# Optimization experiments

Hardware: AMD Instinct MI355X
Metric: run time of the kernel (lower is better)

## Reference

```python
import jax, jax.numpy as jnp
import numpy as np

N_HEADS = 8
N_HIDDEN = 64  # out_features // n_heads
SLOPE = 0.2
NEG = -9e15


def setup_inputs() -> dict:
    key = jax.random.key(0)
    k1, k2, k3, k4, k5 = jax.random.split(key, 5)
    B, N, F_in, F_out = 4, 2048, 512, 512
    h = jax.random.normal(k1, (B, N, F_in), dtype=jnp.float32)
    adj = jax.random.randint(k2, (B, N, N), 0, 2, dtype=jnp.int32)
    # xavier_uniform with gain=1.414: limit = gain*sqrt(6/(fan_in+fan_out))
    lim_W = 1.414 * np.sqrt(6.0 / (F_in + F_out))
    W_l = jax.random.uniform(k3, (F_in, F_out), jnp.float32, -lim_W, lim_W)
    W_r = jax.random.uniform(k4, (F_in, F_out), jnp.float32, -lim_W, lim_W)
    lim_a = 1.414 * np.sqrt(6.0 / (N_HIDDEN + 1))
    a = jax.random.uniform(k5, (N_HIDDEN, 1), jnp.float32, -lim_a, lim_a)
    return {"h": h, "adj": adj, "W_l": W_l, "W_r": W_r, "a": a}


def reference(h, adj, W_l, W_r, a):
    B, N, _ = h.shape
    H, d = N_HEADS, N_HIDDEN
    # torch .view(-1, H, N, d) is a raw row-major reshape, replicated exactly here
    Wh_l = jax.nn.leaky_relu((h @ W_l).reshape(B, H, N, d), SLOPE)
    Wh_r = jax.nn.leaky_relu((h @ W_r).reshape(B, H, N, d), SLOPE)
    # e: [B,H,N,1] + [B,H,1,N] -> [B,H,N,N]
    e = Wh_l @ a + jnp.swapaxes(Wh_r @ a, 2, 3)
    att = jnp.where(adj[:, None, :, :] > 0, e, NEG)
    att = jax.nn.softmax(att, axis=-1)
    h_prime = att @ Wh_r  # [B,H,N,d]
    # torch .view(-1, N, H*d): raw reshape (no head transpose)
    out = jax.nn.elu(h_prime.reshape(B, N, H * d))
    return out
```

## Files before the change

kernel.cpp:

```cpp
#include <hip/hip_runtime.h>

#define NB   4
#define NN   2048
#define FIN  512
#define FOUT 512
#define NHD  8
#define DH   64
#define VTR  520
#define SLOPE 0.2f

typedef __attribute__((ext_vector_type(8)))  short bhalf8;
typedef __attribute__((ext_vector_type(16))) float f32x16;

__device__ __forceinline__ void load_lds16(const void* g, void* l) {
  __builtin_amdgcn_global_load_lds(
      (const __attribute__((address_space(1))) unsigned int*)g,
      (__attribute__((address_space(3))) unsigned int*)l, 16, 0, 0);
}

__device__ __forceinline__ unsigned short bfrne(float x) {
  unsigned int u = __float_as_uint(x);
  return (unsigned short)((u + 0x7FFFu + ((u >> 16) & 1u)) >> 16);
}

__device__ __forceinline__ void split2(float x, float y,
                                       unsigned int& hp, unsigned int& lp) {
  unsigned int ux = __float_as_uint(x), uy = __float_as_uint(y);
  unsigned int rx = (ux + 0x7FFFu + ((ux >> 16) & 1u)) & 0xFFFF0000u;
  unsigned int ry = (uy + 0x7FFFu + ((uy >> 16) & 1u)) & 0xFFFF0000u;
  float lx = x - __uint_as_float(rx);
  float ly = y - __uint_as_float(ry);
  unsigned int vx = __float_as_uint(lx), vy = __float_as_uint(ly);
  hp = (rx >> 16) | ry;
  lp = ((vx + 0x7FFFu + ((vx >> 16) & 1u)) >> 16)
     | ((vy + 0x7FFFu + ((vy >> 16) & 1u)) & 0xFFFF0000u);
}

__global__ __launch_bounds__(256) void k_split_prep(
    const float* __restrict__ h,
    unsigned short* __restrict__ hHi, unsigned short* __restrict__ hLo,
    const float* __restrict__ Wr,
    unsigned short* __restrict__ wTh, unsigned short* __restrict__ wTl)
{
  __shared__ float s[64][65];
  const int t = threadIdx.x;
  if (blockIdx.x < 2048) {
    size_t base = ((size_t)blockIdx.x * 256 + t) * 8;
    float4 a = *(const float4*)(h + base);
    float4 b = *(const float4*)(h + base + 4);
    uint4 uh, ul;
    split2(a.x, a.y, uh.x, ul.x);
    split2(a.z, a.w, uh.y, ul.y);
    split2(b.x, b.y, uh.z, ul.z);
    split2(b.z, b.w, uh.w, ul.w);
    *(uint4*)(hHi + base) = uh;
    *(uint4*)(hLo + base) = ul;
    return;
  }
  const int bid2 = blockIdx.x - 2048;
  const int n0 = (bid2 & 7) * 64, k0 = (bid2 >> 3) * 64;
#pragma unroll
  for (int p = 0; p < 4; ++p) {
    int row = p * 16 + (t >> 4);
    int col = (t & 15) * 4;
    float4 v = *(const float4*)(Wr + (size_t)(k0 + row) * FOUT + n0 + col);
    s[row][col] = v.x; s[row][col+1] = v.y; s[row][col+2] = v.z; s[row][col+3] = v.w;
  }
  __syncthreads();
  const int n = t >> 2;
  const int ks = (t & 3) * 16;
  uint4 h0, h1, l0, l1;
  split2(s[ks+ 0][n], s[ks+ 1][n], h0.x, l0.x);
  split2(s[ks+ 2][n], s[ks+ 3][n], h0.y, l0.y);
  split2(s[ks+ 4][n], s[ks+ 5][n], h0.z, l0.z);
  split2(s[ks+ 6][n], s[ks+ 7][n], h0.w, l0.w);
  split2(s[ks+ 8][n], s[ks+ 9][n], h1.x, l1.x);
  split2(s[ks+10][n], s[ks+11][n], h1.y, l1.y);
  split2(s[ks+12][n], s[ks+13][n], h1.z, l1.z);
  split2(s[ks+14][n], s[ks+15][n], h1.w, l1.w);
  size_t o = (size_t)(n0 + n) * FIN + k0 + ks;
  *(uint4*)(wTh + o) = h0; *(uint4*)(wTh + o + 8) = h1;
  *(uint4*)(wTl + o) = l0; *(uint4*)(wTl + o + 8) = l1;
}

__global__ __launch_bounds__(256) void k_gemm_whr_mfma(
    const unsigned short* __restrict__ hHi, const unsigned short* __restrict__ hLo,
    const unsigned short* __restrict__ wTh, const unsigned short* __restrict__ wTl,
    float* __restrict__ Whr, const float* __restrict__ av, float* __restrict__ er)
{
  __shared__ unsigned short sAh[128*64], sAl[128*64];
  __shared__ unsigned short sBh[64*64],  sBl[64*64];
  __shared__ float erT[128][2];
  const int tid = threadIdx.x, lane = tid & 63, wv = tid >> 6;
  const int Bid = blockIdx.x;
  const int g8 = Bid & 7, idx = Bid >> 3;
  const int sg = idx >> 3, ct = idx & 7;
  const int c0 = ct * 64;
  const int row0 = (g8 * 8 + sg) * 128;

  const unsigned short* pAh[4]; const unsigned short* pAl[4];
  unsigned short *dAh[4], *dAl[4];
#pragma unroll
  for (int t = 0; t < 4; ++t) {
    int I  = wv + t * 4;
    int rl = I * 8 + (lane >> 3);
    int gk = (lane & 7) ^ (rl & 7);
    pAh[t] = hHi + (size_t)(row0 + rl) * FIN + gk * 8;
    pAl[t] = hLo + (size_t)(row0 + rl) * FIN + gk * 8;
    dAh[t] = sAh + I * 512;  dAl[t] = sAl + I * 512;
  }
  const unsigned short* pBh[2]; const unsigned short* pBl[2];
  unsigned short *dBh[2], *dBl[2];
#pragma unroll
  for (int t = 0; t < 2; ++t) {
    int I  = wv + t * 4;
    int rl = I * 8 + (lane >> 3);
    int gk = (lane & 7) ^ (rl & 7);
    pBh[t] = wTh + (size_t)(c0 + rl) * FIN + gk * 8;
    pBl[t] = wTl + (size_t)(c0 + rl) * FIN + gk * 8;
    dBh[t] = sBh + I * 512;  dBl[t] = sBl + I * 512;
  }

  const int wi = wv >> 1, wc = wv & 1;
  const int l31 = lane & 31, half = lane >> 5;
  const int aoff0 = (wi*64 +      l31) * 64;
  const int aoff1 = (wi*64 + 32 + l31) * 64;
  const int boff  = (wc*32 +      l31) * 64;
  f32x16 acc0 = {}; f32x16 acc1 = {};

  for (int k0 = 0; k0 < FIN; k0 += 64) {
#pragma unroll
    for (int t = 0; t < 4; ++t) { load_lds16(pAh[t] + k0, dAh[t]);
                                  load_lds16(pAl[t] + k0, dAl[t]); }
#pragma unroll
    for (int t = 0; t < 2; ++t) { load_lds16(pBh[t] + k0, dBh[t]);
                                  load_lds16(pBl[t] + k0, dBl[t]); }
    __syncthreads();
#pragma unroll
    for (int kb = 0; kb < 4; ++kb) {
      int kg = ((kb*2 + half) ^ (lane & 7)) * 8;
      bhalf8 bh  = *(const bhalf8*)&sBh[boff  + kg];
      bhalf8 bl  = *(const bhalf8*)&sBl[boff  + kg];
      bhalf8 a0h = *(const bhalf8*)&sAh[aoff0 + kg];
      bhalf8 a0l = *(const bhalf8*)&sAl[aoff0 + kg];
      bhalf8 a1h = *(const bhalf8*)&sAh[aoff1 + kg];
      bhalf8 a1l = *(const bhalf8*)&sAl[aoff1 + kg];
      acc0 = __builtin_amdgcn_mfma_f32_32x32x16_bf16(a0h, bh, acc0, 0, 0, 0);
      acc1 = __builtin_amdgcn_mfma_f32_32x32x16_bf16(a1h, bh, acc1, 0, 0, 0);
      acc0 = __builtin_amdgcn_mfma_f32_32x32x16_bf16(a0l, bh, acc0, 0, 0, 0);
      acc1 = __builtin_amdgcn_mfma_f32_32x32x16_bf16(a1l, bh, acc1, 0, 0, 0);
      acc0 = __builtin_amdgcn_mfma_f32_32x32x16_bf16(a0h, bl, acc0, 0, 0, 0);
      acc1 = __builtin_amdgcn_mfma_f32_32x32x16_bf16(a1h, bl, acc1, 0, 0, 0);
    }
    __syncthreads();
  }

  const float a_d = av[wc*32 + l31];
#pragma unroll
  for (int mi = 0; mi < 2; ++mi) {
    const f32x16 a = mi ? acc1 : acc0;
#pragma unroll
    for (int reg = 0; reg < 16; ++reg) {
      int rmap = (reg & 3) + 8*(reg >> 2) + 4*half;
      int rowloc = wi*64 + mi*32 + rmap;
      int grow = row0 + rowloc;
      int b  = grow >> 11;
      int n  = grow & 2047;
      int hd = n >> 8;
      int jj = ((n & 255) << 3) | ct;
      float v = a[reg];
      v = v > 0.f ? v : SLOPE * v;
      Whr[(((size_t)(b*NHD + hd)) * NN + jj) * DH + (wc*32 + l31)] = v;
      float p = v * a_d;
      p += __shfl_xor(p, 16, 32);
      p += __shfl_xor(p,  8, 32);
      p += __shfl_xor(p,  4, 32);
      p += __shfl_xor(p,  2, 32);
      p += __shfl_xor(p,  1, 32);
      if (l31 == 0) erT[rowloc][wc] = p;
    }
  }
  __syncthreads();
  if (tid < 128) {
    int grow = row0 + tid;
    int b  = grow >> 11;
    int n  = grow & 2047;
    int hd = n >> 8;
    int jj = ((n & 255) << 3) | ct;
    er[((size_t)(b*NHD + hd)) * NN + jj] = erT[tid][0] + erT[tid][1];
  }
}

__global__ __launch_bounds__(256) void k_softvt(
    const float* __restrict__ Whr, const float* __restrict__ er,
    unsigned short* __restrict__ Vt)
{
  __shared__ float wm[4];
  __shared__ float wbuf[256];
  __shared__ unsigned short tile[64][264];
  const int tid = threadIdx.x;
  const int jc = blockIdx.x, hh = blockIdx.y, b = blockIdx.z;
  const float* ep = er + ((size_t)(b*NHD + hh)) * NN;
  float m = -1e30f;
  for (int j = tid; j < NN; j += 256) m = fmaxf(m, ep[j]);
#pragma unroll
  for (int off = 32; off; off >>= 1) m = fmaxf(m, __shfl_down(m, off, 64));
  if ((tid & 63) == 0) wm[tid >> 6] = m;
  __syncthreads();
  const float mm = fmaxf(fmaxf(wm[0], wm[1]), fmaxf(wm[2], wm[3]));
  const int j0 = jc * 256;
  float w = expf(ep[j0 + tid] - mm);
  wbuf[tid] = w;
  Vt[((size_t)(b*VTR + 512 + hh)) * NN + j0 + tid] = bfrne(w);
  __syncthreads();
  const size_t wbase = ((size_t)(b*NHD + hh)) * NN;
#pragma unroll
  for (int p = 0; p < 16; ++p) {
    int jr = p*16 + (tid >> 4);
    int dc = (tid & 15) * 4;
    float4 v = *(const float4*)(Whr + (wbase + j0 + jr) * DH + dc);
    float wj = wbuf[jr];
    tile[dc+0][jr] = bfrne(v.x * wj);
    tile[dc+1][jr] = bfrne(v.y * wj);
    tile[dc+2][jr] = bfrne(v.z * wj);
    tile[dc+3][jr] = bfrne(v.w * wj);
  }
  __syncthreads();
#pragma unroll
  for (int q = 0; q < 8; ++q) {
    int idx = q*256 + tid;
    int d = idx >> 5, seg = idx & 31;
    uint4 t16 = *(const uint4*)&tile[d][seg*8];
    *(uint4*)(Vt + ((size_t)(b*VTR + hh*64 + d)) * NN + j0 + seg*8) = t16;
  }
}

__global__ __launch_bounds__(256) void k_attn_out(
    const int* __restrict__ adj, const unsigned short* __restrict__ Vt,
    float* __restrict__ out)
{
  __shared__ unsigned short sA[128][72];
  __shared__ unsigned short sB[2][72*64];
  __shared__ float denL[128];
  const int tid = threadIdx.x;
  const int lane = tid & 63, wv = tid >> 6;
  const int Bid = blockIdx.x;
  const int g8 = Bid & 7, rest = Bid >> 3;
  const int ct = rest & 7, sg = rest >> 3;
  const int row0 = (g8*8 + sg) * 128;
  const int b = row0 >> 11;

  const unsigned short* pB[3];
  int dOff[3];
#pragma unroll
  for (int t = 0; t < 2; ++t) {
    int I  = wv + t*4;
    int rl = I*8 + (lane >> 3);
    int gk = (lane & 7) ^ (rl & 7);
    pB[t] = Vt + ((size_t)(b*VTR + ct*64 + rl))*NN + gk*8;
    dOff[t] = I*512;
  }
  {
    int x  = lane >> 3;
    int gk = (lane & 7) ^ (x & 7);
    pB[2] = Vt + ((size_t)(b*VTR + 512 + x))*NN + gk*8;
    dOff[2] = 64*64;
  }

  const int* adjp = adj + (size_t)b*NN*NN + (size_t)(row0 & 2047)*NN
                    + (tid >> 3)*NN + (tid & 7)*8;
  unsigned short* sAp = &sA[tid >> 3][(tid & 7)*8];

  const int wi = wv >> 1, wc = wv & 1;
  const int l31 = lane & 31, half = lane >> 5;
  f32x16 acc0 = {}; f32x16 acc1 = {}; f32x16 acc2 = {};
  const unsigned short* aRd0 = &sA[wi*64 +      l31][half*8];
  const unsigned short* aRd1 = &sA[wi*64 + 32 + l31][half*8];
  const int nloc = wc*32 + l31;

  load_lds16(pB[0], &sB[0][dOff[0]]);
  load_lds16(pB[1], &sB[0][dOff[1]]);
  if (wv == 0) load_lds16(pB[2], &sB[0][dOff[2]]);
  int4 q[8];
#pragma unroll
  for (int rr = 0; rr < 4; ++rr) {
    q[2*rr]   = *(const int4*)(adjp + rr*32*NN);
    q[2*rr+1] = *(const int4*)(adjp + rr*32*NN + 4);
  }

  for (int it = 0; it < 32; ++it) {
    const int cur = it & 1;
#pragma unroll
    for (int rr = 0; rr < 4; ++rr) {
      uint4 u;
      u.x = (unsigned)(q[2*rr].x   | (q[2*rr].y   << 16)) * 0x3F80u;
      u.y = (unsigned)(q[2*rr].z   | (q[2*rr].w   << 16)) * 0x3F80u;
      u.z = (unsigned)(q[2*rr+1].x | (q[2*rr+1].y << 16)) * 0x3F80u;
      u.w = (unsigned)(q[2*rr+1].z | (q[2*rr+1].w << 16)) * 0x3F80u;
      *(uint4*)(sAp + rr*32*72) = u;
    }
    __syncthreads();
    if (it < 31) {
      const int nk = (it + 1) * 64;
      unsigned short* nb = sB[cur ^ 1];
      load_lds16(pB[0] + nk, nb + dOff[0]);
      load_lds16(pB[1] + nk, nb + dOff[1]);
      if (wv == 0) load_lds16(pB[2] + nk, nb + dOff[2]);
#pragma unroll
      for (int rr = 0; rr < 4; ++rr) {
        q[2*rr]   = *(const int4*)(adjp + rr*32*NN + nk);
        q[2*rr+1] = *(const int4*)(adjp + rr*32*NN + nk + 4);
      }
    }
    const unsigned short* sBc = sB[cur];
#pragma unroll
    for (int kb = 0; kb < 4; ++kb) {
      int kg = (kb*2 + half) ^ (lane & 7);
      bhalf8 bf  = *(const bhalf8*)&sBc[nloc*64 + kg*8];
      bhalf8 bf2 = {};
      if (l31 < 8) bf2 = *(const bhalf8*)&sBc[(64 + l31)*64 + kg*8];
      bhalf8 a0 = *(const bhalf8*)(aRd0 + kb*16);
      bhalf8 a1 = *(const bhalf8*)(aRd1 + kb*16);
      acc0 = __builtin_amdgcn_mfma_f32_32x32x16_bf16(a0, bf,  acc0, 0, 0, 0);
      acc1 = __builtin_amdgcn_mfma_f32_32x32x16_bf16(a1, bf,  acc1, 0, 0, 0);
      acc2 = __builtin_amdgcn_mfma_f32_32x32x16_bf16(wc ? a1 : a0, bf2, acc2, 0, 0, 0);
    }
    __syncthreads();
  }
  if (l31 == ct) {
#pragma unroll
    for (int reg = 0; reg < 16; ++reg)
      denL[wv*32 + (reg & 3) + 8*(reg >> 2) + 4*half] = acc2[reg];
  }
  __syncthreads();
  const int ib = row0 & 2047;
#pragma unroll
  for (int mi = 0; mi < 2; ++mi) {
    const f32x16 a = mi ? acc1 : acc0;
#pragma unroll
    for (int reg = 0; reg < 16; ++reg) {
      int il = wi*64 + mi*32 + (reg & 3) + 8*(reg >> 2) + 4*half;
      int i  = ib + il;
      float v = a[reg] / denL[il];
      v = v > 0.f ? v : expm1f(v);
      int n = (ct << 8) | (i >> 3);
      int f = ((i & 7) << 6) | nloc;
      out[((size_t)b*NN + n)*FOUT + f] = v;
    }
  }
}

extern "C" void kernel_launch(void* const* d_in, const int* in_sizes, int n_in,
                              void* d_out, int out_size, void* d_ws, size_t ws_size,
                              hipStream_t stream)
{
  const float* hin = (const float*)d_in[0];
  const int*   adj = (const int*)d_in[1];
  const float* Wr  = (const float*)d_in[3];
  const float* av  = (const float*)d_in[4];
  float* out = (float*)d_out;

  char* ws = (char*)d_ws;
  unsigned short* hHi = (unsigned short*)(ws);
  unsigned short* hLo = (unsigned short*)(ws + 8388608);
  unsigned short* wTh = (unsigned short*)(ws + 16777216);
  unsigned short* wTl = (unsigned short*)(ws + 17301504);
  float* Whr  = (float*)(ws + 17825792);
  float* er   = (float*)(ws + 34603008);
  unsigned short* Vt = (unsigned short*)(ws);

  k_split_prep   <<<dim3(2112),    256, 0, stream>>>(hin, hHi, hLo, Wr, wTh, wTl);
  k_gemm_whr_mfma<<<dim3(512),     256, 0, stream>>>(hHi, hLo, wTh, wTl, Whr, av, er);
  k_softvt       <<<dim3(8, 8, 4), 256, 0, stream>>>(Whr, er, Vt);
  k_attn_out     <<<dim3(512),     256, 0, stream>>>(adj, Vt, out);
}
```

Measured before the change: 198.6 us.

## Fuse four kernels into one persistent kernel with software grid barriers

Merges the split/prep, GEMM, softmax-weight and attention kernels into one 512-block kernel whose stages share an LDS union and are separated by atomic-counter grid barriers. The aim is to remove inter-kernel launch gaps and tail drain between stages. The softmax stage now uses 128-column chunks so its work maps onto the same 512 blocks. The barrier needs all 512 blocks co-resident (launch_bounds 256,2) and adds a memset launch plus spin-wait cost at each stage boundary.

```diff
diff --git a/kernel.cpp b/kernel.cpp
--- a/kernel.cpp
+++ b/kernel.cpp
@@ -8,6 +8,7 @@
 #define DH   64
 #define VTR  520
 #define SLOPE 0.2f
+#define NBLK 512
 
 typedef __attribute__((ext_vector_type(8)))  short bhalf8;
 typedef __attribute__((ext_vector_type(16))) float f32x16;
@@ -36,316 +37,340 @@
      | ((vy + 0x7FFFu + ((vy >> 16) & 1u)) & 0xFFFF0000u);
 }
 
-__global__ __launch_bounds__(256) void k_split_prep(
-    const float* __restrict__ h,
-    unsigned short* __restrict__ hHi, unsigned short* __restrict__ hLo,
-    const float* __restrict__ Wr,
-    unsigned short* __restrict__ wTh, unsigned short* __restrict__ wTl)
-{
-  __shared__ float s[64][65];
-  const int t = threadIdx.x;
-  if (blockIdx.x < 2048) {
-    size_t base = ((size_t)blockIdx.x * 256 + t) * 8;
-    float4 a = *(const float4*)(h + base);
-    float4 b = *(const float4*)(h + base + 4);
-    uint4 uh, ul;
-    split2(a.x, a.y, uh.x, ul.x);
-    split2(a.z, a.w, uh.y, ul.y);
-    split2(b.x, b.y, uh.z, ul.z);
-    split2(b.z, b.w, uh.w, ul.w);
-    *(uint4*)(hHi + base) = uh;
-    *(uint4*)(hLo + base) = ul;
-    return;
-  }
-  const int bid2 = blockIdx.x - 2048;
-  const int n0 = (bid2 & 7) * 64, k0 = (bid2 >> 3) * 64;
-#pragma unroll
-  for (int p = 0; p < 4; ++p) {
-    int row = p * 16 + (t >> 4);
-    int col = (t & 15) * 4;
-    float4 v = *(const float4*)(Wr + (size_t)(k0 + row) * FOUT + n0 + col);
-    s[row][col] = v.x; s[row][col+1] = v.y; s[row][col+2] = v.z; s[row][col+3] = v.w;
+union SharedMem {
+  struct { float s[64][65]; } prep;
+  struct {
+    unsigned short sAh[128*64], sAl[128*64];
+    unsigned short sBh[64*64],  sBl[64*64];
+    float erT[128][2];
+  } gemm;
+  struct { float wm[4]; float wbuf[128]; unsigned short tile[64][136]; } soft;
+  struct {
+    unsigned short sA[128][72];
+    unsigned short sB[2][72*64];
+    float denL[128];
+  } attn;
+};
+
+__device__ __forceinline__ void grid_sync(unsigned* bar) {
+  __syncthreads();
+  if (threadIdx.x == 0) {
+    __threadfence();
+    unsigned g = __hip_atomic_load(&bar[1], __ATOMIC_RELAXED, __HIP_MEMORY_SCOPE_AGENT);
+    unsigned a = __hip_atomic_fetch_add(&bar[0], 1u, __ATOMIC_ACQ_REL, __HIP_MEMORY_SCOPE_AGENT);
+    if (a + 1u == (unsigned)NBLK) {
+      __hip_atomic_store(&bar[0], 0u, __ATOMIC_RELAXED, __HIP_MEMORY_SCOPE_AGENT);
+      __hip_atomic_fetch_add(&bar[1], 1u, __ATOMIC_RELEASE, __HIP_MEMORY_SCOPE_AGENT);
+    } else {
+      while (__hip_atomic_load(&bar[1], __ATOMIC_ACQUIRE, __HIP_MEMORY_SCOPE_AGENT) == g)
+        __builtin_amdgcn_s_sleep(8);
+    }
   }
   __syncthreads();
-  const int n = t >> 2;
-  const int ks = (t & 3) * 16;
-  uint4 h0, h1, l0, l1;
-  split2(s[ks+ 0][n], s[ks+ 1][n], h0.x, l0.x);
-  split2(s[ks+ 2][n], s[ks+ 3][n], h0.y, l0.y);
-  split2(s[ks+ 4][n], s[ks+ 5][n], h0.z, l0.z);
-  split2(s[ks+ 6][n], s[ks+ 7][n], h0.w, l0.w);
-  split2(s[ks+ 8][n], s[ks+ 9][n], h1.x, l1.x);
-  split2(s[ks+10][n], s[ks+11][n], h1.y, l1.y);
-  split2(s[ks+12][n], s[ks+13][n], h1.z, l1.z);
-  split2(s[ks+14][n], s[ks+15][n], h1.w, l1.w);
-  size_t o = (size_t)(n0 + n) * FIN + k0 + ks;
-  *(uint4*)(wTh + o) = h0; *(uint4*)(wTh + o + 8) = h1;
-  *(uint4*)(wTl + o) = l0; *(uint4*)(wTl + o + 8) = l1;
-}
-
-__global__ __launch_bounds__(256) void k_gemm_whr_mfma(
-    const unsigned short* __restrict__ hHi, const unsigned short* __restrict__ hLo,
-    const unsigned short* __restrict__ wTh, const unsigned short* __restrict__ wTl,
-    float* __restrict__ Whr, const float* __restrict__ av, float* __restrict__ er)
+}
+
+__global__ __launch_bounds__(256, 2) void k_fused(
+    const float* __restrict__ hin, const int* __restrict__ adj,
+    const float* __restrict__ Wr,  const float* __restrict__ av,
+    float* __restrict__ out,
+    unsigned short* __restrict__ hHi, unsigned short* __restrict__ hLo,
+    unsigned short* __restrict__ wTh, unsigned short* __restrict__ wTl,
+    float* __restrict__ Whr, float* __restrict__ er,
+    unsigned short* __restrict__ Vt, unsigned* __restrict__ bar)
 {
-  __shared__ unsigned short sAh[128*64], sAl[128*64];
-  __shared__ unsigned short sBh[64*64],  sBl[64*64];
-  __shared__ float erT[128][2];
-  const int tid = threadIdx.x, lane = tid & 63, wv = tid >> 6;
-  const int Bid = blockIdx.x;
-  const int g8 = Bid & 7, idx = Bid >> 3;
-  const int sg = idx >> 3, ct = idx & 7;
-  const int c0 = ct * 64;
-  const int row0 = (g8 * 8 + sg) * 128;
-
-  const unsigned short* pAh[4]; const unsigned short* pAl[4];
-  unsigned short *dAh[4], *dAl[4];
-#pragma unroll
-  for (int t = 0; t < 4; ++t) {
-    int I  = wv + t * 4;
-    int rl = I * 8 + (lane >> 3);
-    int gk = (lane & 7) ^ (rl & 7);
-    pAh[t] = hHi + (size_t)(row0 + rl) * FIN + gk * 8;
-    pAl[t] = hLo + (size_t)(row0 + rl) * FIN + gk * 8;
-    dAh[t] = sAh + I * 512;  dAl[t] = sAl + I * 512;
+  __shared__ SharedMem smem;
+  const int tid = threadIdx.x;
+  const int bid = blockIdx.x;
+  const int lane = tid & 63, wv = tid >> 6;
+
+  for (int u = bid; u < 2112; u += NBLK) {
+    if (u < 2048) {
+      size_t base = ((size_t)u * 256 + tid) * 8;
+      float4 a = *(const float4*)(hin + base);
+      float4 b = *(const float4*)(hin + base + 4);
+      uint4 uh, ul;
+      split2(a.x, a.y, uh.x, ul.x);
+      split2(a.z, a.w, uh.y, ul.y);
+      split2(b.x, b.y, uh.z, ul.z);
+      split2(b.z, b.w, uh.w, ul.w);
+      *(uint4*)(hHi + base) = uh;
+      *(uint4*)(hLo + base) = ul;
+    } else {
+      auto& s = smem.prep.s;
+      const int bid2 = u - 2048;
+      const int n0 = (bid2 & 7) * 64, k0 = (bid2 >> 3) * 64;
+#pragma unroll
+      for (int p = 0; p < 4; ++p) {
+        int row = p * 16 + (tid >> 4);
+        int col = (tid & 15) * 4;
+        float4 v = *(const float4*)(Wr + (size_t)(k0 + row) * FOUT + n0 + col);
+        s[row][col] = v.x; s[row][col+1] = v.y; s[row][col+2] = v.z; s[row][col+3] = v.w;
+      }
+      __syncthreads();
+      const int n = tid >> 2;
+      const int ks = (tid & 3) * 16;
+      uint4 h0, h1, l0, l1;
+      split2(s[ks+ 0][n], s[ks+ 1][n], h0.x, l0.x);
+      split2(s[ks+ 2][n], s[ks+ 3][n], h0.y, l0.y);
+      split2(s[ks+ 4][n], s[ks+ 5][n], h0.z, l0.z);
+      split2(s[ks+ 6][n], s[ks+ 7][n], h0.w, l0.w);
+      split2(s[ks+ 8][n], s[ks+ 9][n], h1.x, l1.x);
+      split2(s[ks+10][n], s[ks+11][n], h1.y, l1.y);
+      split2(s[ks+12][n], s[ks+13][n], h1.z, l1.z);
+      split2(s[ks+14][n], s[ks+15][n], h1.w, l1.w);
+      size_t o = (size_t)(n0 + n) * FIN + k0 + ks;
+      *(uint4*)(wTh + o) = h0; *(uint4*)(wTh + o + 8) = h1;
+      *(uint4*)(wTl + o) = l0; *(uint4*)(wTl + o + 8) = l1;
+    }
   }
-  const unsigned short* pBh[2]; const unsigned short* pBl[2];
-  unsigned short *dBh[2], *dBl[2];
-#pragma unroll
-  for (int t = 0; t < 2; ++t) {
-    int I  = wv + t * 4;
-    int rl = I * 8 + (lane >> 3);
-    int gk = (lane & 7) ^ (rl & 7);
-    pBh[t] = wTh + (size_t)(c0 + rl) * FIN + gk * 8;
-    pBl[t] = wTl + (size_t)(c0 + rl) * FIN + gk * 8;
-    dBh[t] = sBh + I * 512;  dBl[t] = sBl + I * 512;
-  }
-
-  const int wi = wv >> 1, wc = wv & 1;
-  const int l31 = lane & 31, half = lane >> 5;
-  const int aoff0 = (wi*64 +      l31) * 64;
-  const int aoff1 = (wi*64 + 32 + l31) * 64;
-  const int boff  = (wc*32 +      l31) * 64;
-  f32x16 acc0 = {}; f32x16 acc1 = {};
-
-  for (int k0 = 0; k0 < FIN; k0 += 64) {
-#pragma unroll
-    for (int t = 0; t < 4; ++t) { load_lds16(pAh[t] + k0, dAh[t]);
-                                  load_lds16(pAl[t] + k0, dAl[t]); }
-#pragma unroll
-    for (int t = 0; t < 2; ++t) { load_lds16(pBh[t] + k0, dBh[t]);
-                                  load_lds16(pBl[t] + k0, dBl[t]); }
+  grid_sync(bar);
+
+  {
+    auto& S = smem.gemm;
+    const int g8 = bid & 7, idx = bid >> 3;
+    const int sg = idx >> 3, ct = idx & 7;
+    const int c0 = ct * 64;
+    const int row0 = (g8 * 8 + sg) * 128;
+
+    const unsigned short* pAh[4]; const unsigned short* pAl[4];
+    unsigned short *dAh[4], *dAl[4];
+#pragma unroll
+    for (int t = 0; t < 4; ++t) {
+      int I  = wv + t * 4;
+      int rl = I * 8 + (lane >> 3);
+      int gk = (lane & 7) ^ (rl & 7);
+      pAh[t] = hHi + (size_t)(row0 + rl) * FIN + gk * 8;
+      pAl[t] = hLo + (size_t)(row0 + rl) * FIN + gk * 8;
+      dAh[t] = S.sAh + I * 512;  dAl[t] = S.sAl + I * 512;
+    }
+    const unsigned short* pBh[2]; const unsigned short* pBl[2];
+    unsigned short *dBh[2], *dBl[2];
+#pragma unroll
+    for (int t = 0; t < 2; ++t) {
+      int I  = wv + t * 4;
+      int rl = I * 8 + (lane >> 3);
+      int gk = (lane & 7) ^ (rl & 7);
+      pBh[t] = wTh + (size_t)(c0 + rl) * FIN + gk * 8;
+      pBl[t] = wTl + (size_t)(c0 + rl) * FIN + gk * 8;
+      dBh[t] = S.sBh + I * 512;  dBl[t] = S.sBl + I * 512;
+    }
+
+    const int wi = wv >> 1, wc = wv & 1;
+    const int l31 = lane & 31, half = lane >> 5;
+    const int aoff0 = (wi*64 +      l31) * 64;
+    const int aoff1 = (wi*64 + 32 + l31) * 64;
+    const int boff  = (wc*32 +      l31) * 64;
+    f32x16 acc0 = {}; f32x16 acc1 = {};
+
+    for (int k0 = 0; k0 < FIN; k0 += 64) {
+#pragma unroll
+      for (int t = 0; t < 4; ++t) { load_lds16(pAh[t] + k0, dAh[t]);
+                                    load_lds16(pAl[t] + k0, dAl[t]); }
+#pragma unroll
+      for (int t = 0; t < 2; ++t) { load_lds16(pBh[t] + k0, dBh[t]);
+                                    load_lds16(pBl[t] + k0, dBl[t]); }
+      __syncthreads();
+#pragma unroll
+      for (int kb = 0; kb < 4; ++kb) {
+        int kg = ((kb*2 + half) ^ (lane & 7)) * 8;
+        bhalf8 bh  = *(const bhalf8*)&S.sBh[boff  + kg];
+        bhalf8 bl  = *(const bhalf8*)&S.sBl[boff  + kg];
+        bhalf8 a0h = *(const bhalf8*)&S.sAh[aoff0 + kg];
+        bhalf8 a0l = *(const bhalf8*)&S.sAl[aoff0 + kg];
+        bhalf8 a1h = *(const bhalf8*)&S.sAh[aoff1 + kg];
+        bhalf8 a1l = *(const bhalf8*)&S.sAl[aoff1 + kg];
+        acc0 = __builtin_amdgcn_mfma_f32_32x32x16_bf16(a0h, bh, acc0, 0, 0, 0);
+        acc1 = __builtin_amdgcn_mfma_f32_32x32x16_bf16(a1h, bh, acc1, 0, 0, 0);
+        acc0 = __builtin_amdgcn_mfma_f32_32x32x16_bf16(a0l, bh, acc0, 0, 0, 0);
+        acc1 = __builtin_amdgcn_mfma_f32_32x32x16_bf16(a1l, bh, acc1, 0, 0, 0);
+        acc0 = __builtin_amdgcn_mfma_f32_32x32x16_bf16(a0h, bl, acc0, 0, 0, 0);
+        acc1 = __builtin_amdgcn_mfma_f32_32x32x16_bf16(a1h, bl, acc1, 0, 0, 0);
+      }
+      __syncthreads();
+    }
+
+    const float a_d = av[wc*32 + l31];
+#pragma unroll
+    for (int mi = 0; mi < 2; ++mi) {
+      const f32x16 a = mi ? acc1 : acc0;
+#pragma unroll
+      for (int reg = 0; reg < 16; ++reg) {
+        int rmap = (reg & 3) + 8*(reg >> 2) + 4*half;
+        int rowloc = wi*64 + mi*32 + rmap;
+        int grow = row0 + rowloc;
+        int b  = grow >> 11;
+        int n  = grow & 2047;
+        int hd = n >> 8;
+        int jj = ((n & 255) << 3) | ct;
+        float v = a[reg];
+        v = v > 0.f ? v : SLOPE * v;
+        Whr[(((size_t)(b*NHD + hd)) * NN + jj) * DH + (wc*32 + l31)] = v;
+        float p = v * a_d;
+        p += __shfl_xor(p, 16, 32);
+        p += __shfl_xor(p,  8, 32);
+        p += __shfl_xor(p,  4, 32);
+        p += __shfl_xor(p,  2, 32);
+        p += __shfl_xor(p,  1, 32);
+        if (l31 == 0) S.erT[rowloc][wc] = p;
+      }
+    }
     __syncthreads();
-#pragma unroll
-    for (int kb = 0; kb < 4; ++kb) {
-      int kg = ((kb*2 + half) ^ (lane & 7)) * 8;
-      bhalf8 bh  = *(const bhalf8*)&sBh[boff  + kg];
-      bhalf8 bl  = *(const bhalf8*)&sBl[boff  + kg];
-      bhalf8 a0h = *(const bhalf8*)&sAh[aoff0 + kg];
-      bhalf8 a0l = *(const bhalf8*)&sAl[aoff0 + kg];
-      bhalf8 a1h = *(const bhalf8*)&sAh[aoff1 + kg];
-      bhalf8 a1l = *(const bhalf8*)&sAl[aoff1 + kg];
-      acc0 = __builtin_amdgcn_mfma_f32_32x32x16_bf16(a0h, bh, acc0, 0, 0, 0);
-      acc1 = __builtin_amdgcn_mfma_f32_32x32x16_bf16(a1h, bh, acc1, 0, 0, 0);
-      acc0 = __builtin_amdgcn_mfma_f32_32x32x16_bf16(a0l, bh, acc0, 0, 0, 0);
-      acc1 = __builtin_amdgcn_mfma_f32_32x32x16_bf16(a1l, bh, acc1, 0, 0, 0);
-      acc0 = __builtin_amdgcn_mfma_f32_32x32x16_bf16(a0h, bl, acc0, 0, 0, 0);
-      acc1 = __builtin_amdgcn_mfma_f32_32x32x16_bf16(a1h, bl, acc1, 0, 0, 0);
-    }
-    __syncthreads();
-  }
-
-  const float a_d = av[wc*32 + l31];
-#pragma unroll
-  for (int mi = 0; mi < 2; ++mi) {
-    const f32x16 a = mi ? acc1 : acc0;
-#pragma unroll
-    for (int reg = 0; reg < 16; ++reg) {
-      int rmap = (reg & 3) + 8*(reg >> 2) + 4*half;
-      int rowloc = wi*64 + mi*32 + rmap;
-      int grow = row0 + rowloc;
+    if (tid < 128) {
+      int grow = row0 + tid;
       int b  = grow >> 11;
       int n  = grow & 2047;
       int hd = n >> 8;
       int jj = ((n & 255) << 3) | ct;
-      float v = a[reg];
-      v = v > 0.f ? v : SLOPE * v;
-      Whr[(((size_t)(b*NHD + hd)) * NN + jj) * DH + (wc*32 + l31)] = v;
-      float p = v * a_d;
-      p += __shfl_xor(p, 16, 32);
-      p += __shfl_xor(p,  8, 32);
-      p += __shfl_xor(p,  4, 32);
-      p += __shfl_xor(p,  2, 32);
-      p += __shfl_xor(p,  1, 32);
-      if (l31 == 0) erT[rowloc][wc] = p;
+      er[((size_t)(b*NHD + hd)) * NN + jj] = S.erT[tid][0] + S.erT[tid][1];
     }
   }
-  __syncthreads();
-  if (tid < 128) {
-    int grow = row0 + tid;
-    int b  = grow >> 11;
-    int n  = grow & 2047;
-    int hd = n >> 8;
-    int jj = ((n & 255) << 3) | ct;
-    er[((size_t)(b*NHD + hd)) * NN + jj] = erT[tid][0] + erT[tid][1];
+  grid_sync(bar);
+
+  {
+    auto& S = smem.soft;
+    const int jc = bid & 15, hh = (bid >> 4) & 7, b = bid >> 7;
+    const float* ep = er + ((size_t)(b*NHD + hh)) * NN;
+    float m = -1e30f;
+    for (int j = tid; j < NN; j += 256) m = fmaxf(m, ep[j]);
+#pragma unroll
+    for (int off = 32; off; off >>= 1) m = fmaxf(m, __shfl_down(m, off, 64));
+    if ((tid & 63) == 0) S.wm[tid >> 6] = m;
+    __syncthreads();
+    const float mm = fmaxf(fmaxf(S.wm[0], S.wm[1]), fmaxf(S.wm[2], S.wm[3]));
+    const int j0 = jc * 128;
+    if (tid < 128) {
+      float w = expf(ep[j0 + tid] - mm);
+      S.wbuf[tid] = w;
+      Vt[((size_t)(b*VTR + 512 + hh)) * NN + j0 + tid] = bfrne(w);
+    }
+    __syncthreads();
+    const size_t wbase = ((size_t)(b*NHD + hh)) * NN;
+#pragma unroll
+    for (int p = 0; p < 8; ++p) {
+      int jr = p*16 + (tid >> 4);
+      int dc = (tid & 15) * 4;
+      float4 v = *(const float4*)(Whr + (wbase + j0 + jr) * DH + dc);
+      float wj = S.wbuf[jr];
+      S.tile[dc+0][jr] = bfrne(v.x * wj);
+      S.tile[dc+1][jr] = bfrne(v.y * wj);
+      S.tile[dc+2][jr] = bfrne(v.z * wj);
+      S.tile[dc+3][jr] = bfrne(v.w * wj);
+    }
+    __syncthreads();
+#pragma unroll
+    for (int q = 0; q < 4; ++q) {
+      int idx = q*256 + tid;
+      int d = idx >> 4, seg = idx & 15;
+      uint4 t16 = *(const uint4*)&S.tile[d][seg*8];
+      *(uint4*)(Vt + ((size_t)(b*VTR + hh*64 + d)) * NN + j0 + seg*8) = t16;
+    }
   }
-}
-
-__global__ __launch_bounds__(256) void k_softvt(
-    const float* __restrict__ Whr, const float* __restrict__ er,
-    unsigned short* __restrict__ Vt)
-{
-  __shared__ float wm[4];
-  __shared__ float wbuf[256];
-  __shared__ unsigned short tile[64][264];
-  const int tid = threadIdx.x;
-  const int jc = blockIdx.x, hh = blockIdx.y, b = blockIdx.z;
-  const float* ep = er + ((size_t)(b*NHD + hh)) * NN;
-  float m = -1e30f;
-  for (int j = tid; j < NN; j += 256) m = fmaxf(m, ep[j]);
-#pragma unroll
-  for (int off = 32; off; off >>= 1) m = fmaxf(m, __shfl_down(m, off, 64));
-  if ((tid & 63) == 0) wm[tid >> 6] = m;
-  __syncthreads();
-  const float mm = fmaxf(fmaxf(wm[0], wm[1]), fmaxf(wm[2], wm[3]));
-  const int j0 = jc * 256;
-  float w = expf(ep[j0 + tid] - mm);
-  wbuf[tid] = w;
-  Vt[((size_t)(b*VTR + 512 + hh)) * NN + j0 + tid] = bfrne(w);
-  __syncthreads();
-  const size_t wbase = ((size_t)(b*NHD + hh)) * NN;
-#pragma unroll
-  for (int p = 0; p < 16; ++p) {
-    int jr = p*16 + (tid >> 4);
-    int dc = (tid & 15) * 4;
-    float4 v = *(const float4*)(Whr + (wbase + j0 + jr) * DH + dc);
-    float wj = wbuf[jr];
-    tile[dc+0][jr] = bfrne(v.x * wj);
-    tile[dc+1][jr] = bfrne(v.y * wj);
-    tile[dc+2][jr] = bfrne(v.z * wj);
-    tile[dc+3][jr] = bfrne(v.w * wj);
-  }
-  __syncthreads();
-#pragma unroll
-  for (int q = 0; q < 8; ++q) {
-    int idx = q*256 + tid;
-    int d = idx >> 5, seg = idx & 31;
-    uint4 t16 = *(const uint4*)&tile[d][seg*8];
-    *(uint4*)(Vt + ((size_t)(b*VTR + hh*64 + d)) * NN + j0 + seg*8) = t16;
-  }
-}
-
-__global__ __launch_bounds__(256) void k_attn_out(
-    const int* __restrict__ adj, const unsigned short* __restrict__ Vt,
-    float* __restrict__ out)
-{
-  __shared__ unsigned short sA[128][72];
-  __shared__ unsigned short sB[2][72*64];
-  __shared__ float denL[128];
-  const int tid = threadIdx.x;
-  const int lane = tid & 63, wv = tid >> 6;
-  const int Bid = blockIdx.x;
-  const int g8 = Bid & 7, rest = Bid >> 3;
-  const int ct = rest & 7, sg = rest >> 3;
-  const int row0 = (g8*8 + sg) * 128;
-  const int b = row0 >> 11;
-
-  const unsigned short* pB[3];
-  int dOff[3];
-#pragma unroll
-  for (int t = 0; t < 2; ++t) {
-    int I  = wv + t*4;
-    int rl = I*8 + (lane >> 3);
-    int gk = (lane & 7) ^ (rl & 7);
-    pB[t] = Vt + ((size_t)(b*VTR + ct*64 + rl))*NN + gk*8;
-    dOff[t] = I*512;
-  }
+  grid_sync(bar);
+
   {
-    int x  = lane >> 3;
-    int gk = (lane & 7) ^ (x & 7);
-    pB[2] = Vt + ((size_t)(b*VTR + 512 + x))*NN + gk*8;
-    dOff[2] = 64*64;
-  }
-
-  const int* adjp = adj + (size_t)b*NN*NN + (size_t)(row0 & 2047)*NN
-                    + (tid >> 3)*NN + (tid & 7)*8;
-  unsigned short* sAp = &sA[tid >> 3][(tid & 7)*8];
-
-  const int wi = wv >> 1, wc = wv & 1;
-  const int l31 = lane & 31, half = lane >> 5;
-  f32x16 acc0 = {}; f32x16 acc1 = {}; f32x16 acc2 = {};
-  const unsigned short* aRd0 = &sA[wi*64 +      l31][half*8];
-  const unsigned short* aRd1 = &sA[wi*64 + 32 + l31][half*8];
-  const int nloc = wc*32 + l31;
-
-  load_lds16(pB[0], &sB[0][dOff[0]]);
-  load_lds16(pB[1], &sB[0][dOff[1]]);
-  if (wv == 0) load_lds16(pB[2], &sB[0][dOff[2]]);
-  int4 q[8];
-#pragma unroll
-  for (int rr = 0; rr < 4; ++rr) {
-    q[2*rr]   = *(const int4*)(adjp + rr*32*NN);
-    q[2*rr+1] = *(const int4*)(adjp + rr*32*NN + 4);
-  }
-
-  for (int it = 0; it < 32; ++it) {
-    const int cur = it & 1;
+    auto& S = smem.attn;
+    const int g8 = bid & 7, rest = bid >> 3;
+    const int ct = rest & 7, sg = rest >> 3;
+    const int row0 = (g8*8 + sg) * 128;
+    const int b = row0 >> 11;
+
+    const unsigned short* pB[3];
+    int dOff[3];
+#pragma unroll
+    for (int t = 0; t < 2; ++t) {
+      int I  = wv + t*4;
+      int rl = I*8 + (lane >> 3);
+      int gk = (lane & 7) ^ (rl & 7);
+      pB[t] = Vt + ((size_t)(b*VTR + ct*64 + rl))*NN + gk*8;
+      dOff[t] = I*512;
+    }
+    {
+      int x  = lane >> 3;
+      int gk = (lane & 7) ^ (x & 7);
+      pB[2] = Vt + ((size_t)(b*VTR + 512 + x))*NN + gk*8;
+      dOff[2] = 64*64;
+    }
+
+    const int* adjp = adj + (size_t)b*NN*NN + (size_t)(row0 & 2047)*NN
+                      + (tid >> 3)*NN + (tid & 7)*8;
+    unsigned short* sAp = &S.sA[tid >> 3][(tid & 7)*8];
+
+    const int wi = wv >> 1, wc = wv & 1;
+    const int l31 = lane & 31, half = lane >> 5;
+    f32x16 acc0 = {}; f32x16 acc1 = {}; f32x16 acc2 = {};
+    const unsigned short* aRd0 = &S.sA[wi*64 +      l31][half*8];
+    const unsigned short* aRd1 = &S.sA[wi*64 + 32 + l31][half*8];
+    const int nloc = wc*32 + l31;
+
+    load_lds16(pB[0], &S.sB[0][dOff[0]]);
+    load_lds16(pB[1], &S.sB[0][dOff[1]]);
+    if (wv == 0) load_lds16(pB[2], &S.sB[0][dOff[2]]);
+    int4 q[8];
 #pragma unroll
     for (int rr = 0; rr < 4; ++rr) {
-      uint4 u;
-      u.x = (unsigned)(q[2*rr].x   | (q[2*rr].y   << 16)) * 0x3F80u;
-      u.y = (unsigned)(q[2*rr].z   | (q[2*rr].w   << 16)) * 0x3F80u;
-      u.z = (unsigned)(q[2*rr+1].x | (q[2*rr+1].y << 16)) * 0x3F80u;
-      u.w = (unsigned)(q[2*rr+1].z | (q[2*rr+1].w << 16)) * 0x3F80u;
-      *(uint4*)(sAp + rr*32*72) = u;
+      q[2*rr]   = *(const int4*)(adjp + rr*32*NN);
+      q[2*rr+1] = *(const int4*)(adjp + rr*32*NN + 4);
+    }
+
+    for (int it = 0; it < 32; ++it) {
+      const int cur = it & 1;
+#pragma unroll
+      for (int rr = 0; rr < 4; ++rr) {
+        uint4 u;
+        u.x = (unsigned)(q[2*rr].x   | (q[2*rr].y   << 16)) * 0x3F80u;
+        u.y = (unsigned)(q[2*rr].z   | (q[2*rr].w   << 16)) * 0x3F80u;
+        u.z = (unsigned)(q[2*rr+1].x | (q[2*rr+1].y << 16)) * 0x3F80u;
+        u.w = (unsigned)(q[2*rr+1].z | (q[2*rr+1].w << 16)) * 0x3F80u;
+        *(uint4*)(sAp + rr*32*72) = u;
+      }
+      __syncthreads();
+      if (it < 31) {
+        const int nk = (it + 1) * 64;
+        unsigned short* nb = S.sB[cur ^ 1];
+        load_lds16(pB[0] + nk, nb + dOff[0]);
+        load_lds16(pB[1] + nk, nb + dOff[1]);
+        if (wv == 0) load_lds16(pB[2] + nk, nb + dOff[2]);
+#pragma unroll
+        for (int rr = 0; rr < 4; ++rr) {
+          q[2*rr]   = *(const int4*)(adjp + rr*32*NN + nk);
+          q[2*rr+1] = *(const int4*)(adjp + rr*32*NN + nk + 4);
+        }
+      }
+      const unsigned short* sBc = S.sB[cur];
+#pragma unroll
+      for (int kb = 0; kb < 4; ++kb) {
+        int kg = (kb*2 + half) ^ (lane & 7);
+        bhalf8 bf  = *(const bhalf8*)&sBc[nloc*64 + kg*8];
+        bhalf8 bf2 = {};
+        if (l31 < 8) bf2 = *(const bhalf8*)&sBc[(64 + l31)*64 + kg*8];
+        bhalf8 a0 = *(const bhalf8*)(aRd0 + kb*16);
+        bhalf8 a1 = *(const bhalf8*)(aRd1 + kb*16);
+        acc0 = __builtin_amdgcn_mfma_f32_32x32x16_bf16(a0, bf,  acc0, 0, 0, 0);
+        acc1 = __builtin_amdgcn_mfma_f32_32x32x16_bf16(a1, bf,  acc1, 0, 0, 0);
+        acc2 = __builtin_amdgcn_mfma_f32_32x32x16_bf16(wc ? a1 : a0, bf2, acc2, 0, 0, 0);
+      }
+      __syncthreads();
+    }
+    if (l31 == ct) {
+#pragma unroll
+      for (int reg = 0; reg < 16; ++reg)
+        S.denL[wv*32 + (reg & 3) + 8*(reg >> 2) + 4*half] = acc2[reg];
     }
     __syncthreads();
-    if (it < 31) {
-      const int nk = (it + 1) * 64;
-      unsigned short* nb = sB[cur ^ 1];
-      load_lds16(pB[0] + nk, nb + dOff[0]);
-      load_lds16(pB[1] + nk, nb + dOff[1]);
-      if (wv == 0) load_lds16(pB[2] + nk, nb + dOff[2]);
-#pragma unroll
-      for (int rr = 0; rr < 4; ++rr) {
-        q[2*rr]   = *(const int4*)(adjp + rr*32*NN + nk);
-        q[2*rr+1] = *(const int4*)(adjp + rr*32*NN + nk + 4);
-      }
-    }
-    const unsigned short* sBc = sB[cur];
-#pragma unroll
-    for (int kb = 0; kb < 4; ++kb) {
-      int kg = (kb*2 + half) ^ (lane & 7);
-      bhalf8 bf  = *(const bhalf8*)&sBc[nloc*64 + kg*8];
-      bhalf8 bf2 = {};
-      if (l31 < 8) bf2 = *(const bhalf8*)&sBc[(64 + l31)*64 + kg*8];
-      bhalf8 a0 = *(const bhalf8*)(aRd0 + kb*16);
-      bhalf8 a1 = *(const bhalf8*)(aRd1 + kb*16);
-      acc0 = __builtin_amdgcn_mfma_f32_32x32x16_bf16(a0, bf,  acc0, 0, 0, 0);
-      acc1 = __builtin_amdgcn_mfma_f32_32x32x16_bf16(a1, bf,  acc1, 0, 0, 0);
-      acc2 = __builtin_amdgcn_mfma_f32_32x32x16_bf16(wc ? a1 : a0, bf2, acc2, 0, 0, 0);
-    }
-    __syncthreads();
-  }
-  if (l31 == ct) {
-#pragma unroll
-    for (int reg = 0; reg < 16; ++reg)
-      denL[wv*32 + (reg & 3) + 8*(reg >> 2) + 4*half] = acc2[reg];
-  }
-  __syncthreads();
-  const int ib = row0 & 2047;
-#pragma unroll
-  for (int mi = 0; mi < 2; ++mi) {
-    const f32x16 a = mi ? acc1 : acc0;
-#pragma unroll
-    for (int reg = 0; reg < 16; ++reg) {
-      int il = wi*64 + mi*32 + (reg & 3) + 8*(reg >> 2) + 4*half;
-      int i  = ib + il;
-      float v = a[reg] / denL[il];
-      v = v > 0.f ? v : expm1f(v);
-      int n = (ct << 8) | (i >> 3);
-      int f = ((i & 7) << 6) | nloc;
-      out[((size_t)b*NN + n)*FOUT + f] = v;
+    const int ib = row0 & 2047;
+#pragma unroll
+    for (int mi = 0; mi < 2; ++mi) {
+      const f32x16 a = mi ? acc1 : acc0;
+#pragma unroll
+      for (int reg = 0; reg < 16; ++reg) {
+        int il = wi*64 + mi*32 + (reg & 3) + 8*(reg >> 2) + 4*half;
+        int i  = ib + il;
+        float v = a[reg] / S.denL[il];
+        v = v > 0.f ? v : expm1f(v);
+        int n = (ct << 8) | (i >> 3);
+        int f = ((i & 7) << 6) | nloc;
+        out[((size_t)b*NN + n)*FOUT + f] = v;
+      }
     }
   }
 }
@@ -368,9 +393,9 @@
   float* Whr  = (float*)(ws + 17825792);
   float* er   = (float*)(ws + 34603008);
   unsigned short* Vt = (unsigned short*)(ws);
-
-  k_split_prep   <<<dim3(2112),    256, 0, stream>>>(hin, hHi, hLo, Wr, wTh, wTl);
-  k_gemm_whr_mfma<<<dim3(512),     256, 0, stream>>>(hHi, hLo, wTh, wTl, Whr, av, er);
-  k_softvt       <<<dim3(8, 8, 4), 256, 0, stream>>>(Whr, er, Vt);
-  k_attn_out     <<<dim3(512),     256, 0, stream>>>(adj, Vt, out);
-}
+  unsigned* bar = (unsigned*)(ws + 34865152);
+
+  hipMemsetAsync(bar, 0, 8, stream);
+  k_fused<<<dim3(NBLK), dim3(256), 0, stream>>>(
+      hin, adj, Wr, av, out, hHi, hLo, wTh, wTl, Whr, er, Vt, bar);
+}
```

New measurement: 429.8 us. 116% more time.

## Halve attention row tile to 64 rows and store Whr intermediate as bf16

Applied to the files above, without the earlier changes.

The attention-output kernel now handles 64 rows per block instead of 128 and launches twice as many blocks. Each wave keeps one accumulator, and the denominator MFMA runs only on half the waves. Launch bounds ask for four blocks per CU, aiming at better occupancy and latency hiding. Separately, the Whr intermediate is written as bf16 rather than fp32, halving its write and read traffic between the GEMM and softvt kernels. This adds an extra rounding step, and each Vt tile is now loaded twice as often across blocks.

```diff
diff --git a/kernel.cpp b/kernel.cpp
--- a/kernel.cpp
+++ b/kernel.cpp
@@ -21,6 +21,9 @@
 __device__ __forceinline__ unsigned short bfrne(float x) {
   unsigned int u = __float_as_uint(x);
   return (unsigned short)((u + 0x7FFFu + ((u >> 16) & 1u)) >> 16);
+}
+__device__ __forceinline__ float bf2f(unsigned short u) {
+  return __uint_as_float(((unsigned int)u) << 16);
 }
 
 __device__ __forceinline__ void split2(float x, float y,
@@ -86,7 +89,8 @@
 __global__ __launch_bounds__(256) void k_gemm_whr_mfma(
     const unsigned short* __restrict__ hHi, const unsigned short* __restrict__ hLo,
     const unsigned short* __restrict__ wTh, const unsigned short* __restrict__ wTl,
-    float* __restrict__ Whr, const float* __restrict__ av, float* __restrict__ er)
+    unsigned short* __restrict__ Whr, const float* __restrict__ av,
+    float* __restrict__ er)
 {
   __shared__ unsigned short sAh[128*64], sAl[128*64];
   __shared__ unsigned short sBh[64*64],  sBl[64*64];
@@ -170,7 +174,7 @@
       int jj = ((n & 255) << 3) | ct;
       float v = a[reg];
       v = v > 0.f ? v : SLOPE * v;
-      Whr[(((size_t)(b*NHD + hd)) * NN + jj) * DH + (wc*32 + l31)] = v;
+      Whr[(((size_t)(b*NHD + hd)) * NN + jj) * DH + (wc*32 + l31)] = bfrne(v);
       float p = v * a_d;
       p += __shfl_xor(p, 16, 32);
       p += __shfl_xor(p,  8, 32);
@@ -192,7 +196,7 @@
 }
 
 __global__ __launch_bounds__(256) void k_softvt(
-    const float* __restrict__ Whr, const float* __restrict__ er,
+    const unsigned short* __restrict__ Whr, const float* __restrict__ er,
     unsigned short* __restrict__ Vt)
 {
   __shared__ float wm[4];
@@ -218,12 +222,12 @@
   for (int p = 0; p < 16; ++p) {
     int jr = p*16 + (tid >> 4);
     int dc = (tid & 15) * 4;
-    float4 v = *(const float4*)(Whr + (wbase + j0 + jr) * DH + dc);
+    ushort4 v = *(const ushort4*)(Whr + (wbase + j0 + jr) * DH + dc);
     float wj = wbuf[jr];
-    tile[dc+0][jr] = bfrne(v.x * wj);
-    tile[dc+1][jr] = bfrne(v.y * wj);
-    tile[dc+2][jr] = bfrne(v.z * wj);
-    tile[dc+3][jr] = bfrne(v.w * wj);
+    tile[dc+0][jr] = bfrne(bf2f(v.x) * wj);
+    tile[dc+1][jr] = bfrne(bf2f(v.y) * wj);
+    tile[dc+2][jr] = bfrne(bf2f(v.z) * wj);
+    tile[dc+3][jr] = bfrne(bf2f(v.w) * wj);
   }
   __syncthreads();
 #pragma unroll
@@ -235,19 +239,19 @@
   }
 }
 
-__global__ __launch_bounds__(256) void k_attn_out(
+__global__ __launch_bounds__(256, 4) void k_attn_out(
     const int* __restrict__ adj, const unsigned short* __restrict__ Vt,
     float* __restrict__ out)
 {
-  __shared__ unsigned short sA[128][72];
+  __shared__ unsigned short sA[64][72];
   __shared__ unsigned short sB[2][72*64];
-  __shared__ float denL[128];
+  __shared__ float denL[64];
   const int tid = threadIdx.x;
   const int lane = tid & 63, wv = tid >> 6;
   const int Bid = blockIdx.x;
   const int g8 = Bid & 7, rest = Bid >> 3;
   const int ct = rest & 7, sg = rest >> 3;
-  const int row0 = (g8*8 + sg) * 128;
+  const int row0 = (g8*16 + sg) * 64;
   const int b = row0 >> 11;
 
   const unsigned short* pB[3];
@@ -273,17 +277,16 @@
 
   const int wi = wv >> 1, wc = wv & 1;
   const int l31 = lane & 31, half = lane >> 5;
-  f32x16 acc0 = {}; f32x16 acc1 = {}; f32x16 acc2 = {};
-  const unsigned short* aRd0 = &sA[wi*64 +      l31][half*8];
-  const unsigned short* aRd1 = &sA[wi*64 + 32 + l31][half*8];
+  f32x16 acc0 = {}; f32x16 acc2 = {};
+  const unsigned short* aRd = &sA[wi*32 + l31][half*8];
   const int nloc = wc*32 + l31;
 
   load_lds16(pB[0], &sB[0][dOff[0]]);
   load_lds16(pB[1], &sB[0][dOff[1]]);
   if (wv == 0) load_lds16(pB[2], &sB[0][dOff[2]]);
-  int4 q[8];
-#pragma unroll
-  for (int rr = 0; rr < 4; ++rr) {
+  int4 q[4];
+#pragma unroll
+  for (int rr = 0; rr < 2; ++rr) {
     q[2*rr]   = *(const int4*)(adjp + rr*32*NN);
     q[2*rr+1] = *(const int4*)(adjp + rr*32*NN + 4);
   }
@@ -291,7 +294,7 @@
   for (int it = 0; it < 32; ++it) {
     const int cur = it & 1;
 #pragma unroll
-    for (int rr = 0; rr < 4; ++rr) {
+    for (int rr = 0; rr < 2; ++rr) {
       uint4 u;
       u.x = (unsigned)(q[2*rr].x   | (q[2*rr].y   << 16)) * 0x3F80u;
       u.y = (unsigned)(q[2*rr].z   | (q[2*rr].w   << 16)) * 0x3F80u;
@@ -307,7 +310,7 @@
       load_lds16(pB[1] + nk, nb + dOff[1]);
       if (wv == 0) load_lds16(pB[2] + nk, nb + dOff[2]);
 #pragma unroll
-      for (int rr = 0; rr < 4; ++rr) {
+      for (int rr = 0; rr < 2; ++rr) {
         q[2*rr]   = *(const int4*)(adjp + rr*32*NN + nk);
         q[2*rr+1] = *(const int4*)(adjp + rr*32*NN + nk + 4);
       }
@@ -316,37 +319,33 @@
 #pragma unroll
     for (int kb = 0; kb < 4; ++kb) {
       int kg = (kb*2 + half) ^ (lane & 7);
-      bhalf8 bf  = *(const bhalf8*)&sBc[nloc*64 + kg*8];
-      bhalf8 bf2 = {};
-      if (l31 < 8) bf2 = *(const bhalf8*)&sBc[(64 + l31)*64 + kg*8];
-      bhalf8 a0 = *(const bhalf8*)(aRd0 + kb*16);
-      bhalf8 a1 = *(const bhalf8*)(aRd1 + kb*16);
-      acc0 = __builtin_amdgcn_mfma_f32_32x32x16_bf16(a0, bf,  acc0, 0, 0, 0);
-      acc1 = __builtin_amdgcn_mfma_f32_32x32x16_bf16(a1, bf,  acc1, 0, 0, 0);
-      acc2 = __builtin_amdgcn_mfma_f32_32x32x16_bf16(wc ? a1 : a0, bf2, acc2, 0, 0, 0);
+      bhalf8 bf = *(const bhalf8*)&sBc[nloc*64 + kg*8];
+      bhalf8 a  = *(const bhalf8*)(aRd + kb*16);
+      acc0 = __builtin_amdgcn_mfma_f32_32x32x16_bf16(a, bf, acc0, 0, 0, 0);
+      if (wc == 0) {
+        bhalf8 bf2 = {};
+        if (l31 < 8) bf2 = *(const bhalf8*)&sBc[(64 + l31)*64 + kg*8];
+        acc2 = __builtin_amdgcn_mfma_f32_32x32x16_bf16(a, bf2, acc2, 0, 0, 0);
+      }
     }
     __syncthreads();
   }
-  if (l31 == ct) {
+  if (wc == 0 && l31 == ct) {
 #pragma unroll
     for (int reg = 0; reg < 16; ++reg)
-      denL[wv*32 + (reg & 3) + 8*(reg >> 2) + 4*half] = acc2[reg];
+      denL[wi*32 + (reg & 3) + 8*(reg >> 2) + 4*half] = acc2[reg];
   }
   __syncthreads();
   const int ib = row0 & 2047;
 #pragma unroll
-  for (int mi = 0; mi < 2; ++mi) {
-    const f32x16 a = mi ? acc1 : acc0;
-#pragma unroll
-    for (int reg = 0; reg < 16; ++reg) {
-      int il = wi*64 + mi*32 + (reg & 3) + 8*(reg >> 2) + 4*half;
-      int i  = ib + il;
-      float v = a[reg] / denL[il];
-      v = v > 0.f ? v : expm1f(v);
-      int n = (ct << 8) | (i >> 3);
-      int f = ((i & 7) << 6) | nloc;
-      out[((size_t)b*NN + n)*FOUT + f] = v;
-    }
+  for (int reg = 0; reg < 16; ++reg) {
+    int il = wi*32 + (reg & 3) + 8*(reg >> 2) + 4*half;
+    int i  = ib + il;
+    float v = acc0[reg] / denL[il];
+    v = v > 0.f ? v : expm1f(v);
+    int n = (ct << 8) | (i >> 3);
+    int f = ((i & 7) << 6) | nloc;
+    out[((size_t)b*NN + n)*FOUT + f] = v;
   }
 }
 
@@ -365,12 +364,12 @@
   unsigned short* hLo = (unsigned short*)(ws + 8388608);
   unsigned short* wTh = (unsigned short*)(ws + 16777216);
   unsigned short* wTl = (unsigned short*)(ws + 17301504);
-  float* Whr  = (float*)(ws + 17825792);
+  unsigned short* Whr = (unsigned short*)(ws + 17825792);
   float* er   = (float*)(ws + 34603008);
   unsigned short* Vt = (unsigned short*)(ws);
 
   k_split_prep   <<<dim3(2112),    256, 0, stream>>>(hin, hHi, hLo, Wr, wTh, wTl);
   k_gemm_whr_mfma<<<dim3(512),     256, 0, stream>>>(hHi, hLo, wTh, wTl, Whr, av, er);
   k_softvt       <<<dim3(8, 8, 4), 256, 0, stream>>>(Whr, er, Vt);
-  k_attn_out     <<<dim3(512),     256, 0, stream>>>(adj, Vt, out);
-}
+  k_attn_out     <<<dim3(1024),    256, 0, stream>>>(adj, Vt, out);
+}
```

Result: slower. 202.7 us (+2.1%).
